# Optimization experiments

Measured on AMD Instinct MI355X. Metric: run time of the kernel, lower is better.

The kernel has to match this reference:

```python
import jax, jax.numpy as jnp
import numpy as np


def gcn_conv(h, edge_index, num_nodes):
    # Symmetric-normalized GCN aggregation: out[i] = sum_{(j->i)} h[j] / sqrt(deg(i)*deg(j))
    row, col = edge_index[0], edge_index[1]
    deg = jax.ops.segment_sum(jnp.ones(col.shape, dtype=h.dtype), col, num_segments=num_nodes)
    d_inv_sqrt = jnp.where(deg > 0, jax.lax.rsqrt(jnp.maximum(deg, 1.0)), 0.0)
    w = d_inv_sqrt[row] * d_inv_sqrt[col]           # [E]
    msg = h[row] * w[:, None]                        # [E, D] gather + scale
    return jax.ops.segment_sum(msg, col, num_segments=num_nodes)  # [N, D] scatter-add


def setup_inputs() -> dict:
    key = jax.random.key(0)
    k1, k2, k3, k4 = jax.random.split(key, 4)
    N, E, F_IN, F_HID, F_OUT = 100000, 1600000, 128, 64, 40
    x = jax.random.normal(k1, (N, F_IN), dtype=jnp.float32)
    edge_index = jax.random.randint(k2, (2, E), 0, N, dtype=jnp.int64)
    # xavier_uniform with gain=1.414 (as in reset_parameters); biases zero
    def xavier(k, shape, gain=1.414):
        fan_out, fan_in = shape
        a = gain * np.sqrt(6.0 / (fan_in + fan_out))
        return jax.random.uniform(k, shape, jnp.float32, -a, a)
    W1 = xavier(k3, (F_HID, F_IN))
    b1 = jnp.zeros((F_HID,), dtype=jnp.float32)
    W2 = xavier(k4, (F_OUT, F_HID))
    b2 = jnp.zeros((F_OUT,), dtype=jnp.float32)
    return {"x": x, "edge_index": edge_index, "W1": W1, "b1": b1, "W2": W2, "b2": b2}


def reference(x, edge_index, W1, b1, W2, b2):
    # GNN.forward with num_layers=2, use_mp=True, eval mode (dropout inactive)
    N = x.shape[0]
    h = x @ W1.T                      # [N, nhid]
    h = gcn_conv(h, edge_index, N)
    h = jax.nn.relu(h + b1)
    h = h @ W2.T                      # [N, nclass]
    h = gcn_conv(h, edge_index, N)
    return h + b2
```

## Files before the change

kernel.cpp:

```cpp
#include <hip/hip_runtime.h>
#include <hip/hip_fp16.h>


typedef __attribute__((ext_vector_type(8))) _Float16 half8v;
typedef __attribute__((ext_vector_type(4))) float   float4v;

__global__ void k_binfill(const int* __restrict__ ed,
                          int* __restrict__ gbincnt, unsigned* __restrict__ binbuf,
                          int E, int cap) {
  __shared__ int hist[512];
  __shared__ int cursor[512];
  __shared__ unsigned rec[4096];
  __shared__ unsigned short binv[4096];
  __shared__ int s_is64;
  int t = threadIdx.x;
  hist[t] = 0; hist[t + 256] = 0;
  if (t == 0) s_is64 = 1;
  __syncthreads();
  {
    int any = 0;
    #pragma unroll
    for (int u = 0; u < 8; ++u) {
      int idx = 2 * (t * 8 + u) + 1;
      if (idx < 2 * E && ed[idx] != 0) any = 1;
    }
    if (any) s_is64 = 0;
  }
  __syncthreads();
  const int is64 = s_is64;
  const int base = blockIdx.x * 4096;
  const int nE = min(4096, E - base);
  for (int j = t; j < nE; j += 256) {
    int e = base + j;
    int r = is64 ? ed[2 * e] : ed[e];
    int c = is64 ? ed[2 * (E + e)] : ed[E + e];
    rec[j] = (unsigned)r | ((unsigned)(c & 255) << 17);
    binv[j] = (unsigned short)(c >> 8);
    atomicAdd(&hist[c >> 8], 1);
  }
  __syncthreads();
  for (int b = t; b < 512; b += 256) {
    int h = hist[b];
    cursor[b] = h ? atomicAdd(&gbincnt[b], h) : 0;
  }
  __syncthreads();
  for (int j = t; j < nE; j += 256) {
    int bin = binv[j];
    int pos = atomicAdd(&cursor[bin], 1);
    if (pos < cap)
      binbuf[(size_t)bin * cap + pos] = rec[j];
  }
}

__global__ void k_degscat(const unsigned* __restrict__ binbuf, const int* __restrict__ gbincnt,
                          float* __restrict__ dis, int* __restrict__ rowptr,
                          int* __restrict__ srcs, int NBINS, int N, int cap) {
  __shared__ int sd[512];
  __shared__ int cnt[256];
  __shared__ int sc[256];
  __shared__ int bc[256][8];
  __shared__ unsigned rec[8192];
  int t = threadIdx.x, b = blockIdx.x;
  sd[t]       = (t < NBINS)       ? min(gbincnt[t], cap)       : 0;
  sd[t + 256] = (t + 256 < NBINS) ? min(gbincnt[t + 256], cap) : 0;
  cnt[t] = 0;
  #pragma unroll
  for (int k = 0; k < 8; ++k) bc[t][k] = 0;
  __syncthreads();
  for (int off = 1; off < 512; off <<= 1) {
    int v0 = (t >= off) ? sd[t - off] : 0;
    int v1 = sd[t + 256 - off];
    __syncthreads();
    sd[t] += v0; sd[t + 256] += v1;
    __syncthreads();
  }
  const int mybase = (b == 0) ? 0 : sd[b - 1];
  if (b == NBINS - 1 && t == 0) rowptr[N] = sd[NBINS - 1];

  int n = min(gbincnt[b], cap);
  const unsigned* buf = binbuf + (size_t)b * cap;
  for (int j = t; j < n; j += 256) {
    unsigned v = buf[j];
    rec[j] = v;
    atomicAdd(&cnt[v >> 17], 1);
    atomicAdd(&bc[v >> 17][(v & 0x1FFFF) >> 14], 1);
  }
  __syncthreads();
  sc[t] = cnt[t];
  __syncthreads();
  for (int off = 1; off < 256; off <<= 1) {
    int v = (t >= off) ? sc[t - off] : 0;
    __syncthreads();
    sc[t] += v;
    __syncthreads();
  }
  int rp = mybase + ((t == 0) ? 0 : sc[t - 1]);
  int node = b * 256 + t;
  if (node < N) {
    int d = cnt[t];
    dis[node] = (d > 0) ? rsqrtf((float)d) : 0.f;
    rowptr[node] = rp;
  }
  {
    int base2 = rp;
    #pragma unroll
    for (int k = 0; k < 8; ++k) {
      int c = bc[t][k];
      bc[t][k] = base2;
      base2 += c;
    }
  }
  __syncthreads();
  for (int j = t; j < n; j += 256) {
    unsigned v = rec[j];
    int pos = atomicAdd(&bc[v >> 17][(v & 0x1FFFF) >> 14], 1);
    srcs[pos] = (int)(v & 0x1FFFF);
  }
}

__launch_bounds__(256)
__global__ void k_gemm1_mfma(const float* __restrict__ X, const float* __restrict__ W,
                             const float* __restrict__ dis, unsigned char* __restrict__ h1q,
                             float* __restrict__ sc1, int N) {
  __shared__ _Float16 wl[64 * 128];
  const int t = threadIdx.x;
  const int row0 = blockIdx.x * 128;
  const int w = t >> 6, l = t & 63;
  const int m0 = w * 32;
  const int lr = l & 15, q = l >> 4;

  float4 xr[4][2][2];
  #pragma unroll
  for (int kc = 0; kc < 4; ++kc) {
    #pragma unroll
    for (int mt = 0; mt < 2; ++mt) {
      int row = min(row0 + m0 + mt * 16 + lr, N - 1);
      const float* p = &X[(size_t)row * 128 + kc * 32 + q * 8];
      xr[kc][mt][0] = *(const float4*)p;
      xr[kc][mt][1] = *(const float4*)(p + 4);
    }
  }

  #pragma unroll
  for (int j = 0; j < 8; ++j) {
    int qq = t + 256 * j;
    int r = qq >> 5, k4 = qq & 31;
    float4 v = *(const float4*)&W[(size_t)r * 128 + k4 * 4];
    _Float16 h4[4] = {(_Float16)v.x, (_Float16)v.y, (_Float16)v.z, (_Float16)v.w};
    int k = (k4 * 4) ^ ((r & 7) * 8);
    *(float2*)&wl[r * 128 + k] = *(float2*)h4;
  }
  __syncthreads();

  float4v acc[2][4] = {};
  #pragma unroll
  for (int kc = 0; kc < 4; ++kc) {
    half8v a[2], b[4];
    #pragma unroll
    for (int mt = 0; mt < 2; ++mt) {
      float4 v0 = xr[kc][mt][0], v1 = xr[kc][mt][1];
      _Float16 h8[8] = {(_Float16)v0.x, (_Float16)v0.y, (_Float16)v0.z, (_Float16)v0.w,
                        (_Float16)v1.x, (_Float16)v1.y, (_Float16)v1.z, (_Float16)v1.w};
      a[mt] = *(half8v*)h8;
    }
    #pragma unroll
    for (int nt = 0; nt < 4; ++nt) {
      int n = nt * 16 + lr;
      int k = (kc * 32 + q * 8) ^ ((n & 7) * 8);
      b[nt] = *(half8v*)&wl[n * 128 + k];
    }
    #pragma unroll
    for (int mt = 0; mt < 2; ++mt)
      #pragma unroll
      for (int nt = 0; nt < 4; ++nt)
        acc[mt][nt] = __builtin_amdgcn_mfma_f32_16x16x32_f16(a[mt], b[nt], acc[mt][nt], 0, 0, 0);
  }

  #pragma unroll
  for (int mt = 0; mt < 2; ++mt) {
    #pragma unroll
    for (int r = 0; r < 4; ++r) {
      int row = row0 + m0 + mt * 16 + q * 4 + r;
      if (row < N) {
        float dr = dis[row];
        float v0 = acc[mt][0][r] * dr;
        float v1 = acc[mt][1][r] * dr;
        float v2 = acc[mt][2][r] * dr;
        float v3 = acc[mt][3][r] * dr;
        float m = fmaxf(fmaxf(fabsf(v0), fabsf(v1)), fmaxf(fabsf(v2), fabsf(v3)));
        #pragma unroll
        for (int off = 1; off < 16; off <<= 1)
          m = fmaxf(m, __shfl_xor(m, off));
        float inv = (m > 0.f) ? (127.f / m) : 0.f;
        unsigned char* dst = h1q + (size_t)row * 64;
        int q0 = (int)rintf(v0 * inv);
        int q1 = (int)rintf(v1 * inv);
        int q2 = (int)rintf(v2 * inv);
        int q3 = (int)rintf(v3 * inv);
        q0 = max(-127, min(127, q0));
        q1 = max(-127, min(127, q1));
        q2 = max(-127, min(127, q2));
        q3 = max(-127, min(127, q3));
        dst[lr]      = (unsigned char)(signed char)q0;
        dst[lr + 16] = (unsigned char)(signed char)q1;
        dst[lr + 32] = (unsigned char)(signed char)q2;
        dst[lr + 48] = (unsigned char)(signed char)q3;
        if (lr == 0) sc1[row] = m * (1.f / 127.f);
      }
    }
  }
}

__launch_bounds__(256)
__global__ void k_gemm2_mfma(const __half* __restrict__ Xh, const float* __restrict__ W,
                             const float* __restrict__ dis, unsigned char* __restrict__ h2,
                             int N) {
  __shared__ _Float16 xl[128 * 64];
  __shared__ _Float16 wl[48 * 64];
  const int t = threadIdx.x;
  const int row0 = blockIdx.x * 128;

  for (int i = t; i < 48 * 8; i += 256) {
    int c = i >> 3, kq = i & 7;
    _Float16 h8[8];
    #pragma unroll
    for (int j = 0; j < 8; ++j)
      h8[j] = (c < 40) ? (_Float16)W[c * 64 + kq * 8 + j] : (_Float16)0.f;
    *(float4*)&wl[c * 64 + ((kq * 8) ^ ((c & 7) * 8))] = *(float4*)h8;
  }
  for (int i = t; i < 1024; i += 256) {
    int r = i >> 3, kq = i & 7;
    int row = row0 + r;
    float4 v = make_float4(0.f, 0.f, 0.f, 0.f);
    if (row < N) v = *(const float4*)&Xh[(size_t)row * 64 + kq * 8];
    *(float4*)&xl[r * 64 + ((kq * 8) ^ ((r & 7) * 8))] = v;
  }
  __syncthreads();

  const int w = t >> 6, l = t & 63;
  const int m0 = w * 32;
  const int lr = l & 15, q = l >> 4;

  float4v acc[2][3] = {};
  #pragma unroll
  for (int kc = 0; kc < 2; ++kc) {
    half8v a[2], b[3];
    #pragma unroll
    for (int mt = 0; mt < 2; ++mt) {
      int m = m0 + mt * 16 + lr;
      int k = (kc * 32 + q * 8) ^ ((m & 7) * 8);
      a[mt] = *(half8v*)&xl[m * 64 + k];
    }
    #pragma unroll
    for (int nt = 0; nt < 3; ++nt) {
      int n = nt * 16 + lr;
      int k = (kc * 32 + q * 8) ^ ((n & 7) * 8);
      b[nt] = *(half8v*)&wl[n * 64 + k];
    }
    #pragma unroll
    for (int mt = 0; mt < 2; ++mt)
      #pragma unroll
      for (int nt = 0; nt < 3; ++nt)
        acc[mt][nt] = __builtin_amdgcn_mfma_f32_16x16x32_f16(a[mt], b[nt], acc[mt][nt], 0, 0, 0);
  }

  #pragma unroll
  for (int mt = 0; mt < 2; ++mt) {
    #pragma unroll
    for (int r = 0; r < 4; ++r) {
      int row = row0 + m0 + mt * 16 + q * 4 + r;
      if (row < N) {
        float dr = dis[row];
        float v0 = acc[mt][0][r] * dr;
        float v1 = acc[mt][1][r] * dr;
        float v2 = acc[mt][2][r] * dr;
        float m = fmaxf(fabsf(v0), fmaxf(fabsf(v1), fabsf(v2)));
        #pragma unroll
        for (int off = 1; off < 16; off <<= 1)
          m = fmaxf(m, __shfl_xor(m, off));
        float s = m * (1.f / 127.f);
        float inv = (m > 0.f) ? (127.f / m) : 0.f;
        unsigned char* dst = h2 + (size_t)row * 64;
        int q0 = (int)rintf(v0 * inv);
        int q1 = (int)rintf(v1 * inv);
        int q2 = (int)rintf(v2 * inv);
        q0 = max(-127, min(127, q0));
        q1 = max(-127, min(127, q1));
        q2 = max(-127, min(127, q2));
        dst[lr]      = (unsigned char)(signed char)q0;
        dst[lr + 16] = (unsigned char)(signed char)q1;
        if (lr + 32 < 40) dst[lr + 32] = (unsigned char)(signed char)q2;
        if (lr == 0) *(float*)&dst[40] = s;
        if (lr >= 1 && lr <= 5) *(int*)&dst[40 + 4 * lr] = 0;
      }
    }
  }
}

__launch_bounds__(256)
__global__ void k_conv64(const unsigned char* __restrict__ H, const float* __restrict__ sc1,
                         const int* __restrict__ rowptr, const int* __restrict__ srcs,
                         const float* __restrict__ dis, const float* __restrict__ b1,
                         __half* __restrict__ out, int N) {
  int t = threadIdx.x;
  int li = t & 7;
  int node = blockIdx.x * 32 + (t >> 3);
  if (node >= N) return;
  int s = rowptr[node], e = rowptr[node + 1];
  int last = e - 1;
  float a0 = 0.f, a1 = 0.f, a2 = 0.f, a3 = 0.f,
        a4 = 0.f, a5 = 0.f, a6 = 0.f, a7 = 0.f;
  for (int p = s; p < e; p += 8) {
    int sv[8]; uint2 rv[8]; float cv[8];
    #pragma unroll
    for (int u = 0; u < 8; ++u) sv[u] = srcs[min(p + u, last)];
    #pragma unroll
    for (int u = 0; u < 8; ++u) rv[u] = *(const uint2*)&H[(size_t)sv[u] * 64 + 8 * li];
    #pragma unroll
    for (int u = 0; u < 8; ++u) cv[u] = sc1[sv[u]];
    #pragma unroll
    for (int u = 0; u < 8; ++u) {
      if (p + u < e) {
        int x0 = (int)rv[u].x, x1 = (int)rv[u].y;
        float c = cv[u];
        a0 = fmaf((float)((x0 << 24) >> 24), c, a0);
        a1 = fmaf((float)((x0 << 16) >> 24), c, a1);
        a2 = fmaf((float)((x0 << 8)  >> 24), c, a2);
        a3 = fmaf((float)( x0        >> 24), c, a3);
        a4 = fmaf((float)((x1 << 24) >> 24), c, a4);
        a5 = fmaf((float)((x1 << 16) >> 24), c, a5);
        a6 = fmaf((float)((x1 << 8)  >> 24), c, a6);
        a7 = fmaf((float)( x1        >> 24), c, a7);
      }
    }
  }
  float dn = dis[node];
  const float* bb = b1 + 8 * li;
  __half hv[8];
  hv[0] = __float2half_rn(fmaxf(fmaf(a0, dn, bb[0]), 0.f));
  hv[1] = __float2half_rn(fmaxf(fmaf(a1, dn, bb[1]), 0.f));
  hv[2] = __float2half_rn(fmaxf(fmaf(a2, dn, bb[2]), 0.f));
  hv[3] = __float2half_rn(fmaxf(fmaf(a3, dn, bb[3]), 0.f));
  hv[4] = __float2half_rn(fmaxf(fmaf(a4, dn, bb[4]), 0.f));
  hv[5] = __float2half_rn(fmaxf(fmaf(a5, dn, bb[5]), 0.f));
  hv[6] = __float2half_rn(fmaxf(fmaf(a6, dn, bb[6]), 0.f));
  hv[7] = __float2half_rn(fmaxf(fmaf(a7, dn, bb[7]), 0.f));
  *(float4*)&out[(size_t)node * 64 + 8 * li] = *(float4*)hv;
}

__launch_bounds__(256)
__global__ void k_conv40(const unsigned char* __restrict__ H, const int* __restrict__ rowptr,
                         const int* __restrict__ srcs, const float* __restrict__ dis,
                         const float* __restrict__ b2, float* __restrict__ out, int N) {
  int t = threadIdx.x;
  int li = t & 7;
  int node = blockIdx.x * 32 + (t >> 3);
  if (node >= N) return;
  bool act = li < 5;
  int s = rowptr[node], e = rowptr[node + 1];
  int last = e - 1;
  float a0 = 0.f, a1 = 0.f, a2 = 0.f, a3 = 0.f,
        a4 = 0.f, a5 = 0.f, a6 = 0.f, a7 = 0.f;
  for (int p = s; p < e; p += 8) {
    int sv[8];
    #pragma unroll
    for (int u = 0; u < 8; ++u) sv[u] = srcs[min(p + u, last)];
    if (act) {
      uint2 rv[8]; float cv[8];
      #pragma unroll
      for (int u = 0; u < 8; ++u)
        rv[u] = *(const uint2*)&H[(size_t)sv[u] * 64 + 8 * li];
      #pragma unroll
      for (int u = 0; u < 8; ++u)
        cv[u] = *(const float*)&H[(size_t)sv[u] * 64 + 40];
      #pragma unroll
      for (int u = 0; u < 8; ++u) {
        if (p + u < e) {
          int x0 = (int)rv[u].x, x1 = (int)rv[u].y;
          float c = cv[u];
          a0 = fmaf((float)((x0 << 24) >> 24), c, a0);
          a1 = fmaf((float)((x0 << 16) >> 24), c, a1);
          a2 = fmaf((float)((x0 << 8)  >> 24), c, a2);
          a3 = fmaf((float)( x0        >> 24), c, a3);
          a4 = fmaf((float)((x1 << 24) >> 24), c, a4);
          a5 = fmaf((float)((x1 << 16) >> 24), c, a5);
          a6 = fmaf((float)((x1 << 8)  >> 24), c, a6);
          a7 = fmaf((float)( x1        >> 24), c, a7);
        }
      }
    }
  }
  if (act) {
    float dn = dis[node];
    const float* bb = b2 + 8 * li;
    float4 v0 = make_float4(fmaf(a0, dn, bb[0]), fmaf(a1, dn, bb[1]),
                            fmaf(a2, dn, bb[2]), fmaf(a3, dn, bb[3]));
    float4 v1 = make_float4(fmaf(a4, dn, bb[4]), fmaf(a5, dn, bb[5]),
                            fmaf(a6, dn, bb[6]), fmaf(a7, dn, bb[7]));
    *(float4*)&out[(size_t)node * 40 + 8 * li] = v0;
    *(float4*)&out[(size_t)node * 40 + 8 * li + 4] = v1;
  }
}

extern "C" void kernel_launch(void* const* d_in, const int* in_sizes, int n_in,
                              void* d_out, int out_size, void* d_ws, size_t ws_size,
                              hipStream_t stream) {
  const float* x  = (const float*)d_in[0];
  const int*   ed = (const int*)d_in[1];
  const float* W1 = (const float*)d_in[2];
  const float* b1 = (const float*)d_in[3];
  const float* W2 = (const float*)d_in[4];
  const float* b2 = (const float*)d_in[5];
  float* out = (float*)d_out;

  const int FIN = 128, FH = 64;
  const int N = in_sizes[0] / FIN;
  const int E = in_sizes[1] / 2;
  const int NBINS = (N + 255) >> 8;

  char* ws = (char*)d_ws;
  size_t off = 0;
  auto alloc = [&](size_t bytes) {
    void* p = ws + off;
    off = (off + bytes + 255) & ~(size_t)255;
    return p;
  };
  int*           gbincnt = (int*)alloc(512 * 4);
  float*         dis     = (float*)alloc((size_t)N * 4);
  int*           rowptr  = (int*)alloc(((size_t)N + 1) * 4);
  int*           srcs    = (int*)alloc((size_t)E * 4);
  unsigned char* h1q     = (unsigned char*)alloc((size_t)N * FH * 2);
  __half*        h1b     = (__half*)alloc((size_t)N * FH * 2);
  unsigned char* h2      = (unsigned char*)alloc((size_t)N * 64);
  float* sc1 = (float*)(h1q + (((size_t)N * 64 + 255) & ~(size_t)255));
  int cap = (int)(((size_t)N * FH * 2) / ((size_t)NBINS * 4));
  if (cap > 8192) cap = 8192;
  unsigned* binbuf = (unsigned*)h1q;

  hipMemsetAsync(gbincnt, 0, 512 * 4, stream);

  int fb = (E + 4095) / 4096;
  k_binfill<<<fb, 256, 0, stream>>>(ed, gbincnt, binbuf, E, cap);
  k_degscat<<<NBINS, 256, 0, stream>>>(binbuf, gbincnt, dis, rowptr, srcs, NBINS, N, cap);

  int mb = (N + 127) / 128;
  int cb = (N + 31) / 32;
  k_gemm1_mfma<<<mb, 256, 0, stream>>>(x, W1, dis, h1q, sc1, N);
  k_conv64<<<cb, 256, 0, stream>>>(h1q, sc1, rowptr, srcs, dis, b1, h1b, N);
  k_gemm2_mfma<<<mb, 256, 0, stream>>>(h1b, W2, dis, h2, N);
  k_conv40<<<cb, 256, 0, stream>>>(h2, rowptr, srcs, dis, b2, out, N);
}
```

Measured before the change: 217.1 us.

## Fuse edge binning with first GEMM in one launch and defer degree scaling

Merges the edge-binning kernel and the first feature-transform GEMM into a single launch whose blocks split by index, so the two independent stages run concurrently. The GEMM no longer waits on degrees: it quantizes unscaled rows, and the degree kernel later multiplies the per-row quantization scale by the inverse sqrt degree. This needs a separate bin buffer instead of aliasing the quantized-feature memory, which raises workspace use and memory traffic. Shared memory is sized to the larger of the two bodies, which may lower occupancy for the GEMM blocks.

```diff
diff --git a/kernel.cpp b/kernel.cpp
--- a/kernel.cpp
+++ b/kernel.cpp
@@ -5,17 +5,18 @@
 typedef __attribute__((ext_vector_type(8))) _Float16 half8v;
 typedef __attribute__((ext_vector_type(4))) float   float4v;
 
-__global__ void k_binfill(const int* __restrict__ ed,
-                          int* __restrict__ gbincnt, unsigned* __restrict__ binbuf,
-                          int E, int cap) {
-  __shared__ int hist[512];
-  __shared__ int cursor[512];
-  __shared__ unsigned rec[4096];
-  __shared__ unsigned short binv[4096];
-  __shared__ int s_is64;
+__device__ __forceinline__ void binfill_body(char* smem, const int* __restrict__ ed,
+                                             int* __restrict__ gbincnt,
+                                             unsigned* __restrict__ binbuf,
+                                             int E, int cap, int bid) {
+  int*            hist   = (int*)smem;
+  int*            cursor = hist + 512;
+  unsigned*       rec    = (unsigned*)(cursor + 512);
+  unsigned short* binv   = (unsigned short*)(rec + 4096);
+  int*            s_is64 = (int*)(binv + 4096);
   int t = threadIdx.x;
   hist[t] = 0; hist[t + 256] = 0;
-  if (t == 0) s_is64 = 1;
+  if (t == 0) *s_is64 = 1;
   __syncthreads();
   {
     int any = 0;
@@ -24,11 +25,11 @@
       int idx = 2 * (t * 8 + u) + 1;
       if (idx < 2 * E && ed[idx] != 0) any = 1;
     }
-    if (any) s_is64 = 0;
-  }
-  __syncthreads();
-  const int is64 = s_is64;
-  const int base = blockIdx.x * 4096;
+    if (any) *s_is64 = 0;
+  }
+  __syncthreads();
+  const int is64 = *s_is64;
+  const int base = bid * 4096;
   const int nE = min(4096, E - base);
   for (int j = t; j < nE; j += 256) {
     int e = base + j;
@@ -52,79 +53,13 @@
   }
 }
 
-__global__ void k_degscat(const unsigned* __restrict__ binbuf, const int* __restrict__ gbincnt,
-                          float* __restrict__ dis, int* __restrict__ rowptr,
-                          int* __restrict__ srcs, int NBINS, int N, int cap) {
-  __shared__ int sd[512];
-  __shared__ int cnt[256];
-  __shared__ int sc[256];
-  __shared__ int bc[256][8];
-  __shared__ unsigned rec[8192];
-  int t = threadIdx.x, b = blockIdx.x;
-  sd[t]       = (t < NBINS)       ? min(gbincnt[t], cap)       : 0;
-  sd[t + 256] = (t + 256 < NBINS) ? min(gbincnt[t + 256], cap) : 0;
-  cnt[t] = 0;
-  #pragma unroll
-  for (int k = 0; k < 8; ++k) bc[t][k] = 0;
-  __syncthreads();
-  for (int off = 1; off < 512; off <<= 1) {
-    int v0 = (t >= off) ? sd[t - off] : 0;
-    int v1 = sd[t + 256 - off];
-    __syncthreads();
-    sd[t] += v0; sd[t + 256] += v1;
-    __syncthreads();
-  }
-  const int mybase = (b == 0) ? 0 : sd[b - 1];
-  if (b == NBINS - 1 && t == 0) rowptr[N] = sd[NBINS - 1];
-
-  int n = min(gbincnt[b], cap);
-  const unsigned* buf = binbuf + (size_t)b * cap;
-  for (int j = t; j < n; j += 256) {
-    unsigned v = buf[j];
-    rec[j] = v;
-    atomicAdd(&cnt[v >> 17], 1);
-    atomicAdd(&bc[v >> 17][(v & 0x1FFFF) >> 14], 1);
-  }
-  __syncthreads();
-  sc[t] = cnt[t];
-  __syncthreads();
-  for (int off = 1; off < 256; off <<= 1) {
-    int v = (t >= off) ? sc[t - off] : 0;
-    __syncthreads();
-    sc[t] += v;
-    __syncthreads();
-  }
-  int rp = mybase + ((t == 0) ? 0 : sc[t - 1]);
-  int node = b * 256 + t;
-  if (node < N) {
-    int d = cnt[t];
-    dis[node] = (d > 0) ? rsqrtf((float)d) : 0.f;
-    rowptr[node] = rp;
-  }
-  {
-    int base2 = rp;
-    #pragma unroll
-    for (int k = 0; k < 8; ++k) {
-      int c = bc[t][k];
-      bc[t][k] = base2;
-      base2 += c;
-    }
-  }
-  __syncthreads();
-  for (int j = t; j < n; j += 256) {
-    unsigned v = rec[j];
-    int pos = atomicAdd(&bc[v >> 17][(v & 0x1FFFF) >> 14], 1);
-    srcs[pos] = (int)(v & 0x1FFFF);
-  }
-}
-
-__launch_bounds__(256)
-__global__ void k_gemm1_mfma(const float* __restrict__ X, const float* __restrict__ W,
-                             const float* __restrict__ dis, unsigned char* __restrict__ h1q,
-                             float* __restrict__ sc1, int N) {
-  __shared__ _Float16 wl[64 * 128];
+__device__ __forceinline__ void gemm1_body(char* smem, const float* __restrict__ X,
+                                           const float* __restrict__ W,
+                                           unsigned char* __restrict__ h1q,
+                                           float* __restrict__ sc1, int N, int bid) {
+  _Float16* wl = (_Float16*)smem;
   const int t = threadIdx.x;
-  const int row0 = blockIdx.x * 128;
+  const int row0 = bid * 128;
   const int w = t >> 6, l = t & 63;
   const int m0 = w * 32;
   const int lr = l & 15, q = l >> 4;
@@ -182,11 +117,10 @@
     for (int r = 0; r < 4; ++r) {
       int row = row0 + m0 + mt * 16 + q * 4 + r;
       if (row < N) {
-        float dr = dis[row];
-        float v0 = acc[mt][0][r] * dr;
-        float v1 = acc[mt][1][r] * dr;
-        float v2 = acc[mt][2][r] * dr;
-        float v3 = acc[mt][3][r] * dr;
+        float v0 = acc[mt][0][r];
+        float v1 = acc[mt][1][r];
+        float v2 = acc[mt][2][r];
+        float v3 = acc[mt][3][r];
         float m = fmaxf(fmaxf(fabsf(v0), fabsf(v1)), fmaxf(fabsf(v2), fabsf(v3)));
         #pragma unroll
         for (int off = 1; off < 16; off <<= 1)
@@ -208,6 +142,88 @@
         if (lr == 0) sc1[row] = m * (1.f / 127.f);
       }
     }
+  }
+}
+
+__launch_bounds__(256)
+__global__ void k_prep(const int* __restrict__ ed, int* __restrict__ gbincnt,
+                       unsigned* __restrict__ binbuf, int E, int cap,
+                       const float* __restrict__ X, const float* __restrict__ W,
+                       unsigned char* __restrict__ h1q, float* __restrict__ sc1,
+                       int N, int FB) {
+  __shared__ __align__(16) char smem[28680];
+  if (blockIdx.x < FB)
+    binfill_body(smem, ed, gbincnt, binbuf, E, cap, blockIdx.x);
+  else
+    gemm1_body(smem, X, W, h1q, sc1, N, blockIdx.x - FB);
+}
+
+__global__ void k_degscat(const unsigned* __restrict__ binbuf, const int* __restrict__ gbincnt,
+                          float* __restrict__ dis, int* __restrict__ rowptr,
+                          int* __restrict__ srcs, float* __restrict__ sc1,
+                          int NBINS, int N, int cap) {
+  __shared__ int sd[512];
+  __shared__ int cnt[256];
+  __shared__ int sc[256];
+  __shared__ int bc[256][8];
+  __shared__ unsigned rec[8192];
+  int t = threadIdx.x, b = blockIdx.x;
+  sd[t]       = (t < NBINS)       ? min(gbincnt[t], cap)       : 0;
+  sd[t + 256] = (t + 256 < NBINS) ? min(gbincnt[t + 256], cap) : 0;
+  cnt[t] = 0;
+  #pragma unroll
+  for (int k = 0; k < 8; ++k) bc[t][k] = 0;
+  __syncthreads();
+  for (int off = 1; off < 512; off <<= 1) {
+    int v0 = (t >= off) ? sd[t - off] : 0;
+    int v1 = sd[t + 256 - off];
+    __syncthreads();
+    sd[t] += v0; sd[t + 256] += v1;
+    __syncthreads();
+  }
+  const int mybase = (b == 0) ? 0 : sd[b - 1];
+  if (b == NBINS - 1 && t == 0) rowptr[N] = sd[NBINS - 1];
+
+  int n = min(gbincnt[b], cap);
+  const unsigned* buf = binbuf + (size_t)b * cap;
+  for (int j = t; j < n; j += 256) {
+    unsigned v = buf[j];
+    rec[j] = v;
+    atomicAdd(&cnt[v >> 17], 1);
+    atomicAdd(&bc[v >> 17][(v & 0x1FFFF) >> 14], 1);
+  }
+  __syncthreads();
+  sc[t] = cnt[t];
+  __syncthreads();
+  for (int off = 1; off < 256; off <<= 1) {
+    int v = (t >= off) ? sc[t - off] : 0;
+    __syncthreads();
+    sc[t] += v;
+    __syncthreads();
+  }
+  int rp = mybase + ((t == 0) ? 0 : sc[t - 1]);
+  int node = b * 256 + t;
+  if (node < N) {
+    int d = cnt[t];
+    float dv = (d > 0) ? rsqrtf((float)d) : 0.f;
+    dis[node] = dv;
+    rowptr[node] = rp;
+    sc1[node] *= dv;
+  }
+  {
+    int base2 = rp;
+    #pragma unroll
+    for (int k = 0; k < 8; ++k) {
+      int c = bc[t][k];
+      bc[t][k] = base2;
+      base2 += c;
+    }
+  }
+  __syncthreads();
+  for (int j = t; j < n; j += 256) {
+    unsigned v = rec[j];
+    int pos = atomicAdd(&bc[v >> 17][(v & 0x1FFFF) >> 14], 1);
+    srcs[pos] = (int)(v & 0x1FFFF);
   }
 }
 
@@ -417,6 +433,7 @@
   const int N = in_sizes[0] / FIN;
   const int E = in_sizes[1] / 2;
   const int NBINS = (N + 255) >> 8;
+  const int cap = 8192;
 
   char* ws = (char*)d_ws;
   size_t off = 0;
@@ -429,23 +446,20 @@
   float*         dis     = (float*)alloc((size_t)N * 4);
   int*           rowptr  = (int*)alloc(((size_t)N + 1) * 4);
   int*           srcs    = (int*)alloc((size_t)E * 4);
-  unsigned char* h1q     = (unsigned char*)alloc((size_t)N * FH * 2);
+  unsigned*      binbuf  = (unsigned*)alloc((size_t)NBINS * cap * 4);
+  unsigned char* h1q     = (unsigned char*)alloc((size_t)N * 64);
+  float*         sc1     = (float*)alloc((size_t)N * 4);
   __half*        h1b     = (__half*)alloc((size_t)N * FH * 2);
   unsigned char* h2      = (unsigned char*)alloc((size_t)N * 64);
-  float* sc1 = (float*)(h1q + (((size_t)N * 64 + 255) & ~(size_t)255));
-  int cap = (int)(((size_t)N * FH * 2) / ((size_t)NBINS * 4));
-  if (cap > 8192) cap = 8192;
-  unsigned* binbuf = (unsigned*)h1q;
 
   hipMemsetAsync(gbincnt, 0, 512 * 4, stream);
 
   int fb = (E + 4095) / 4096;
-  k_binfill<<<fb, 256, 0, stream>>>(ed, gbincnt, binbuf, E, cap);
-  k_degscat<<<NBINS, 256, 0, stream>>>(binbuf, gbincnt, dis, rowptr, srcs, NBINS, N, cap);
-
   int mb = (N + 127) / 128;
   int cb = (N + 31) / 32;
-  k_gemm1_mfma<<<mb, 256, 0, stream>>>(x, W1, dis, h1q, sc1, N);
+  k_prep<<<fb + mb, 256, 0, stream>>>(ed, gbincnt, binbuf, E, cap, x, W1, h1q, sc1, N, fb);
+  k_degscat<<<NBINS, 256, 0, stream>>>(binbuf, gbincnt, dis, rowptr, srcs, sc1,
+                                       NBINS, N, cap);
   k_conv64<<<cb, 256, 0, stream>>>(h1q, sc1, rowptr, srcs, dis, b1, h1b, N);
   k_gemm2_mfma<<<mb, 256, 0, stream>>>(h1b, W2, dis, h2, N);
   k_conv40<<<cb, 256, 0, stream>>>(h2, rowptr, srcs, dis, b2, out, N);
```

After: 210.6 us (median of 2 runs). 1.03x faster.
